# Kernel tuning notes

Measured on AMD Instinct MI355X. Metric: run time of the kernel, lower is better.

Reference implementation:

```python
import jax, jax.numpy as jnp
import numpy as np

B, N, L, D = 128, 1024, 512, 64


def setup_inputs() -> dict:
    key = jax.random.key(0)
    k1, k2 = jax.random.split(key)
    text_outputs = jax.random.normal(k1, (B, N, D), dtype=jnp.float32)
    image_outputs = jax.random.normal(k2, (B, L, D), dtype=jnp.float32)
    rng = np.random.RandomState(0)
    ntok = rng.randint(N // 4, N + 1, size=B)
    nreg = rng.randint(L // 4, L + 1, size=B)
    text_mask = (np.arange(N)[None, :] < ntok[:, None]).astype(np.float32)
    image_mask = (np.arange(L)[None, :] < nreg[:, None]).astype(np.float32)
    # impostor indices (torch code samples these with np.random inside forward;
    # here they are fixed constants for determinism), guaranteed != own index
    I_imp = rng.randint(0, B, size=B)
    S_imp = rng.randint(0, B, size=B)
    ar = np.arange(B)
    I_imp = np.where(I_imp == ar, (I_imp + 1) % B, I_imp).astype(np.int32)
    S_imp = np.where(S_imp == ar, (S_imp + 1) % B, S_imp).astype(np.int32)
    return {
        "text_outputs": text_outputs,
        "image_outputs": image_outputs,
        "text_mask": jnp.asarray(text_mask),
        "image_mask": jnp.asarray(image_mask),
        "I_imp_idx": jnp.asarray(I_imp),
        "S_imp_idx": jnp.asarray(S_imp),
    }


def _mean_max_sim(T, I, tmask, imask):
    # T: (N, D) tokens, I: (L, D) regions; masks select the ragged valid prefix.
    M = jnp.einsum('nd,ld->nl', T, I)                       # matchmap (N, L)
    neg = jnp.finfo(M.dtype).min
    mx = jnp.max(jnp.where(imask[None, :] > 0, M, neg), axis=1)  # max over regions
    return jnp.sum(mx * tmask) / jnp.sum(tmask)             # mean over valid tokens


def reference(text_outputs, image_outputs, text_mask, image_mask, I_imp_idx, S_imp_idx, margin=1.0):
    sim = jax.vmap(_mean_max_sim)
    anchor = sim(text_outputs, image_outputs, text_mask, image_mask)            # (B,)
    Simpsim = sim(text_outputs[S_imp_idx], image_outputs, text_mask[S_imp_idx], image_mask)
    Iimpsim = sim(text_outputs, image_outputs[I_imp_idx], text_mask, image_mask[I_imp_idx])
    # scalar per-sample hinge: term added only when margin+imp-anchor > 0 == relu
    per_sample = jax.nn.relu(margin + Iimpsim - anchor) + jax.nn.relu(margin + Simpsim - anchor)
    loss = jnp.sum(per_sample) / text_outputs.shape[0]
    return loss[None]  # torch returns shape (1,)
```

## Files before the change

kernel.cpp:

```cpp
#include <hip/hip_runtime.h>
#include <hip/hip_bf16.h>

#define B 128
#define N 1024
#define L 512
#define D 64
#define TT 6
#define TOKBLK 384
#define NCH 3

typedef float f32x4 __attribute__((ext_vector_type(4)));
typedef short bf16x8 __attribute__((ext_vector_type(8)));

__device__ inline bf16x8 cvt8(float4 f0, float4 f1) {
    union { __hip_bfloat162 h2[4]; bf16x8 v; } u;
    u.h2[0] = __float22bfloat162_rn(make_float2(f0.x, f0.y));
    u.h2[1] = __float22bfloat162_rn(make_float2(f0.z, f0.w));
    u.h2[2] = __float22bfloat162_rn(make_float2(f1.x, f1.y));
    u.h2[3] = __float22bfloat162_rn(make_float2(f1.z, f1.w));
    return u.v;
}

#define WS_NEED_PRE (8192 + (size_t)B * L * D * 2)

__global__ __launch_bounds__(256) void prep_kernel(
        const float* __restrict__ I, const float* __restrict__ tmask,
        const float* __restrict__ imask, unsigned short* __restrict__ Ibf,
        int* __restrict__ cnts) {
    int blk = blockIdx.x;
    int tid = threadIdx.x;
    __shared__ float red[4];
    if (blk < 1024) {
        const float* src = I + (size_t)blk * 64 * D;
        unsigned short* dst = Ibf + (size_t)blk * 4096;
#pragma unroll
        for (int j = 0; j < 2; ++j) {
            int si = tid + j * 256;
            int r = si >> 3, seg = si & 7;
            const float4* p = (const float4*)(src + (size_t)si * 8);
            bf16x8 v = cvt8(p[0], p[1]);
            int h = seg >> 2, qq = seg & 3;
            int ci = ((r >> 4) * 2 + h) * 64 + qq * 16 + (r & 15);
            *(bf16x8*)(dst + (size_t)ci * 8) = v;
        }
    } else {
        int row = blk - 1024;
        float s = 0.f;
        if (row < B) {
            const float* p = tmask + (size_t)row * N;
            for (int i = tid; i < N; i += 256) s += p[i];
        } else {
            const float* p = imask + (size_t)(row - B) * L;
            for (int i = tid; i < L; i += 256) s += p[i];
        }
        for (int off = 32; off > 0; off >>= 1) s += __shfl_down(s, off);
        if ((tid & 63) == 0) red[tid >> 6] = s;
        __syncthreads();
        if (tid == 0)
            cnts[row] = (int)(red[0] + red[1] + red[2] + red[3] + 0.5f);
    }
}

template <bool PRE>
__global__ __launch_bounds__(256, 4) void sim_kernel(
        const float* __restrict__ T, const float* __restrict__ I,
        const unsigned short* __restrict__ Ibf, const int* __restrict__ cnts,
        const int* __restrict__ Iimp, const int* __restrict__ Simp,
        float* __restrict__ partials) {
    int blk = blockIdx.x;
    int chunk = blk % NCH;
    int bs = blk / NCH;
    int b = bs & (B - 1);
    int s = bs >> 7;
    int Tb = b, Ib = b;
    if (s == 1) Tb = Simp[b];
    else if (s == 2) Ib = Iimp[b];
    int ntok = cnts[Tb];
    int nreg = cnts[B + Ib];

    int tid = threadIdx.x;
    int tok0 = chunk * TOKBLK;
    if (tok0 >= ntok) {
        if (tid == 0) partials[blk] = 0.f;
        return;
    }

    int w = tid >> 6;
    int lane = tid & 63;
    int q = lane >> 4;
    int c = lane & 15;

    __shared__ float wsum[4];

    int wt0 = tok0 + w * (TT * 16);
    bf16x8 afrag[TT][2];
#pragma unroll
    for (int tt = 0; tt < TT; ++tt) {
        int row = wt0 + tt * 16 + c;
        if (row > N - 1) row = N - 1;
        const float* trow = T + ((size_t)Tb * N + row) * D;
#pragma unroll
        for (int h = 0; h < 2; ++h) {
            const float4* p = (const float4*)(trow + h * 32 + q * 8);
            afrag[tt][h] = cvt8(p[0], p[1]);
        }
    }

    float mx[TT][4];
#pragma unroll
    for (int tt = 0; tt < TT; ++tt)
#pragma unroll
        for (int i = 0; i < 4; ++i) mx[tt][i] = -3.0e38f;

    int nrt = (nreg + 15) >> 4;
    int prem = nreg & 15;

    if (PRE) {
        const char* imgL = (const char*)(Ibf + (size_t)Ib * L * D) + (size_t)lane * 16;
        bf16x8 c0 = *(const bf16x8*)(imgL);
        bf16x8 c1 = *(const bf16x8*)(imgL + 1024);
        int r1 = (nrt > 1) ? 1 : 0;
        bf16x8 n0 = *(const bf16x8*)(imgL + (size_t)r1 * 2048);
        bf16x8 n1 = *(const bf16x8*)(imgL + (size_t)r1 * 2048 + 1024);
#pragma unroll 1
        for (int rt = 0; rt < nrt; ++rt) {
            int rp = (rt + 2 < nrt) ? rt + 2 : rt;
            const char* pp = imgL + (size_t)rp * 2048;
            bf16x8 f0 = *(const bf16x8*)(pp);
            bf16x8 f1 = *(const bf16x8*)(pp + 1024);
            bool vld = (rt + 1 < nrt) || (prem == 0) || (c < prem);
#pragma unroll
            for (int tt = 0; tt < TT; ++tt) {
                f32x4 acc = {0.f, 0.f, 0.f, 0.f};
                acc = __builtin_amdgcn_mfma_f32_16x16x32_bf16(afrag[tt][0], c0, acc, 0, 0, 0);
                acc = __builtin_amdgcn_mfma_f32_16x16x32_bf16(afrag[tt][1], c1, acc, 0, 0, 0);
                if (vld) {
#pragma unroll
                    for (int i = 0; i < 4; ++i) mx[tt][i] = fmaxf(mx[tt][i], acc[i]);
                }
            }
            c0 = n0; c1 = n1; n0 = f0; n1 = f1;
        }
    } else {
        const float* Ibase = I + (size_t)Ib * L * D;
#pragma unroll 1
        for (int rt = 0; rt < nrt; ++rt) {
            int r = rt * 16 + c;
            const float4* p0 = (const float4*)(Ibase + (size_t)r * D + q * 8);
            bf16x8 b0 = cvt8(p0[0], p0[1]);
            const float4* p1 = (const float4*)(Ibase + (size_t)r * D + 32 + q * 8);
            bf16x8 b1 = cvt8(p1[0], p1[1]);
            bool vld = (rt + 1 < nrt) || (prem == 0) || (c < prem);
#pragma unroll
            for (int tt = 0; tt < TT; ++tt) {
                f32x4 acc = {0.f, 0.f, 0.f, 0.f};
                acc = __builtin_amdgcn_mfma_f32_16x16x32_bf16(afrag[tt][0], b0, acc, 0, 0, 0);
                acc = __builtin_amdgcn_mfma_f32_16x16x32_bf16(afrag[tt][1], b1, acc, 0, 0, 0);
                if (vld) {
#pragma unroll
                    for (int i = 0; i < 4; ++i) mx[tt][i] = fmaxf(mx[tt][i], acc[i]);
                }
            }
        }
    }

#pragma unroll
    for (int m = 1; m < 16; m <<= 1) {
#pragma unroll
        for (int tt = 0; tt < TT; ++tt)
#pragma unroll
            for (int i = 0; i < 4; ++i)
                mx[tt][i] = fmaxf(mx[tt][i], __shfl_xor(mx[tt][i], m));
    }

    float bsum = 0.f;
    if (c == 0) {
#pragma unroll
        for (int tt = 0; tt < TT; ++tt)
#pragma unroll
            for (int i = 0; i < 4; ++i) {
                int row = wt0 + tt * 16 + q * 4 + i;
                if (row < ntok) bsum += mx[tt][i];
            }
    }
    for (int off = 32; off > 0; off >>= 1) bsum += __shfl_down(bsum, off);
    if (lane == 0) wsum[w] = bsum;
    __syncthreads();
    if (tid == 0)
        partials[blk] = (wsum[0] + wsum[1] + wsum[2] + wsum[3]) / (float)ntok;
}

__global__ void loss_kernel(const float* __restrict__ partials,
                            float* __restrict__ out) {
    int tid = threadIdx.x;
    __shared__ float simsL[384];
    __shared__ float w6[6];
    simsL[tid] = partials[tid * NCH] + partials[tid * NCH + 1] + partials[tid * NCH + 2];
    __syncthreads();
    float per = 0.f;
    if (tid < B) {
        float anc  = simsL[tid];
        float simp = simsL[B + tid];
        float iimp = simsL[2 * B + tid];
        per = fmaxf(1.f + iimp - anc, 0.f) + fmaxf(1.f + simp - anc, 0.f);
    }
    for (int off = 32; off > 0; off >>= 1) per += __shfl_down(per, off);
    if ((tid & 63) == 0) w6[tid >> 6] = per;
    __syncthreads();
    if (tid == 0)
        out[0] = (w6[0] + w6[1] + w6[2] + w6[3] + w6[4] + w6[5]) / (float)B;
}

extern "C" void kernel_launch(void* const* d_in, const int* in_sizes, int n_in,
                              void* d_out, int out_size, void* d_ws, size_t ws_size,
                              hipStream_t stream) {
    const float* T     = (const float*)d_in[0];
    const float* I     = (const float*)d_in[1];
    const float* tmask = (const float*)d_in[2];
    const float* imask = (const float*)d_in[3];
    const int*   Iimp  = (const int*)d_in[4];
    const int*   Simp  = (const int*)d_in[5];

    float* partials = (float*)d_ws;
    int*   cnts     = (int*)((char*)d_ws + 6144);
    unsigned short* Ibf = (unsigned short*)((char*)d_ws + 8192);

    prep_kernel<<<1024 + 2 * B, 256, 0, stream>>>(I, tmask, imask, Ibf, cnts);
    if (ws_size >= WS_NEED_PRE) {
        sim_kernel<true><<<3 * B * NCH, 256, 0, stream>>>(T, I, Ibf, cnts, Iimp, Simp, partials);
    } else {
        sim_kernel<false><<<3 * B * NCH, 256, 0, stream>>>(T, I, Ibf, cnts, Iimp, Simp, partials);
    }
    loss_kernel<<<1, 384, 0, stream>>>(partials, (float*)d_out);
}
```

Measured before the change: 128.1 us.

## Pre-convert text to bf16 fragments and split regions across waves

Result: no change. 129.5 us (+1.1%).

```diff
diff --git a/kernel.cpp b/kernel.cpp
--- a/kernel.cpp
+++ b/kernel.cpp
@@ -5,9 +5,7 @@
 #define N 1024
 #define L 512
 #define D 64
-#define TT 6
-#define TOKBLK 384
-#define NCH 3
+#define NCH 8
 
 typedef float f32x4 __attribute__((ext_vector_type(4)));
 typedef short bf16x8 __attribute__((ext_vector_type(8)));
@@ -21,18 +19,23 @@
     return u.v;
 }
 
-#define WS_NEED_PRE (8192 + (size_t)B * L * D * 2)
+#define TBF_OFF 16384
+#define IBF_OFF (16384 + 16777216)
+#define WS_NEED (IBF_OFF + (size_t)B * L * D * 2)
 
 __global__ __launch_bounds__(256) void prep_kernel(
-        const float* __restrict__ I, const float* __restrict__ tmask,
-        const float* __restrict__ imask, unsigned short* __restrict__ Ibf,
+        const float* __restrict__ T, const float* __restrict__ I,
+        const float* __restrict__ tmask, const float* __restrict__ imask,
+        unsigned short* __restrict__ Tbf, unsigned short* __restrict__ Ibf,
         int* __restrict__ cnts) {
     int blk = blockIdx.x;
     int tid = threadIdx.x;
     __shared__ float red[4];
-    if (blk < 1024) {
-        const float* src = I + (size_t)blk * 64 * D;
-        unsigned short* dst = Ibf + (size_t)blk * 4096;
+    if (blk < 3072) {
+        const float* src;
+        unsigned short* dst;
+        if (blk < 2048) { src = T + (size_t)blk * 64 * D; dst = Tbf + (size_t)blk * 4096; }
+        else { src = I + (size_t)(blk - 2048) * 64 * D; dst = Ibf + (size_t)(blk - 2048) * 4096; }
 #pragma unroll
         for (int j = 0; j < 2; ++j) {
             int si = tid + j * 256;
@@ -44,7 +47,7 @@
             *(bf16x8*)(dst + (size_t)ci * 8) = v;
         }
     } else {
-        int row = blk - 1024;
+        int row = blk - 3072;
         float s = 0.f;
         if (row < B) {
             const float* p = tmask + (size_t)row * N;
@@ -64,12 +67,13 @@
 template <bool PRE>
 __global__ __launch_bounds__(256, 4) void sim_kernel(
         const float* __restrict__ T, const float* __restrict__ I,
-        const unsigned short* __restrict__ Ibf, const int* __restrict__ cnts,
+        const unsigned short* __restrict__ Tbf, const unsigned short* __restrict__ Ibf,
+        const int* __restrict__ cnts,
         const int* __restrict__ Iimp, const int* __restrict__ Simp,
         float* __restrict__ partials) {
     int blk = blockIdx.x;
-    int chunk = blk % NCH;
-    int bs = blk / NCH;
+    int chunk = blk & (NCH - 1);
+    int bs = blk >> 3;
     int b = bs & (B - 1);
     int s = bs >> 7;
     int Tb = b, Ib = b;
@@ -79,7 +83,7 @@
     int nreg = cnts[B + Ib];
 
     int tid = threadIdx.x;
-    int tok0 = chunk * TOKBLK;
+    int tok0 = chunk * 128;
     if (tok0 >= ntok) {
         if (tid == 0) partials[blk] = 0.f;
         return;
@@ -89,105 +93,125 @@
     int lane = tid & 63;
     int q = lane >> 4;
     int c = lane & 15;
-
-    __shared__ float wsum[4];
-
-    int wt0 = tok0 + w * (TT * 16);
-    bf16x8 afrag[TT][2];
-#pragma unroll
-    for (int tt = 0; tt < TT; ++tt) {
-        int row = wt0 + tt * 16 + c;
-        if (row > N - 1) row = N - 1;
-        const float* trow = T + ((size_t)Tb * N + row) * D;
-#pragma unroll
-        for (int h = 0; h < 2; ++h) {
-            const float4* p = (const float4*)(trow + h * 32 + q * 8);
-            afrag[tt][h] = cvt8(p[0], p[1]);
-        }
-    }
-
-    float mx[TT][4];
-#pragma unroll
-    for (int tt = 0; tt < TT; ++tt)
+    int th = w >> 1;
+    int rh = w & 1;
+
+    __shared__ float ldsmx[2][2][64];
+    __shared__ float wsumS[2];
+
+    int wt0 = tok0 + th * 64;
+    bool active = wt0 < ntok;
+
+    float mx[4][4];
+#pragma unroll
+    for (int tt = 0; tt < 4; ++tt)
 #pragma unroll
         for (int i = 0; i < 4; ++i) mx[tt][i] = -3.0e38f;
 
     int nrt = (nreg + 15) >> 4;
     int prem = nreg & 15;
 
-    if (PRE) {
-        const char* imgL = (const char*)(Ibf + (size_t)Ib * L * D) + (size_t)lane * 16;
-        bf16x8 c0 = *(const bf16x8*)(imgL);
-        bf16x8 c1 = *(const bf16x8*)(imgL + 1024);
-        int r1 = (nrt > 1) ? 1 : 0;
-        bf16x8 n0 = *(const bf16x8*)(imgL + (size_t)r1 * 2048);
-        bf16x8 n1 = *(const bf16x8*)(imgL + (size_t)r1 * 2048 + 1024);
+    if (active) {
+        bf16x8 afrag[4][2];
+        if (PRE) {
+            const char* tb = (const char*)Tbf + (size_t)Tb * 131072
+                           + (size_t)(chunk * 8 + th * 4) * 2048 + (size_t)lane * 16;
+#pragma unroll
+            for (int tt = 0; tt < 4; ++tt)
+#pragma unroll
+                for (int h = 0; h < 2; ++h)
+                    afrag[tt][h] = *(const bf16x8*)(tb + tt * 2048 + h * 1024);
+        } else {
+#pragma unroll
+            for (int tt = 0; tt < 4; ++tt) {
+                const float* trow = T + ((size_t)Tb * N + wt0 + tt * 16 + c) * D;
+#pragma unroll
+                for (int h = 0; h < 2; ++h) {
+                    const float4* p = (const float4*)(trow + h * 32 + q * 8);
+                    afrag[tt][h] = cvt8(p[0], p[1]);
+                }
+            }
+        }
+
+        if (PRE) {
+            const char* imgL = (const char*)Ibf + (size_t)Ib * 65536 + (size_t)lane * 16;
+            bf16x8 c0 = {0}, c1 = {0}, n0 = {0}, n1 = {0};
+            if (rh < nrt) {
+                c0 = *(const bf16x8*)(imgL + (size_t)rh * 2048);
+                c1 = *(const bf16x8*)(imgL + (size_t)rh * 2048 + 1024);
+            }
 #pragma unroll 1
-        for (int rt = 0; rt < nrt; ++rt) {
-            int rp = (rt + 2 < nrt) ? rt + 2 : rt;
-            const char* pp = imgL + (size_t)rp * 2048;
-            bf16x8 f0 = *(const bf16x8*)(pp);
-            bf16x8 f1 = *(const bf16x8*)(pp + 1024);
-            bool vld = (rt + 1 < nrt) || (prem == 0) || (c < prem);
-#pragma unroll
-            for (int tt = 0; tt < TT; ++tt) {
-                f32x4 acc = {0.f, 0.f, 0.f, 0.f};
-                acc = __builtin_amdgcn_mfma_f32_16x16x32_bf16(afrag[tt][0], c0, acc, 0, 0, 0);
-                acc = __builtin_amdgcn_mfma_f32_16x16x32_bf16(afrag[tt][1], c1, acc, 0, 0, 0);
-                if (vld) {
-#pragma unroll
-                    for (int i = 0; i < 4; ++i) mx[tt][i] = fmaxf(mx[tt][i], acc[i]);
-                }
-            }
-            c0 = n0; c1 = n1; n0 = f0; n1 = f1;
-        }
-    } else {
-        const float* Ibase = I + (size_t)Ib * L * D;
+            for (int rt = rh; rt < nrt; rt += 2) {
+                int rn = rt + 2;
+                if (rn < nrt) {
+                    n0 = *(const bf16x8*)(imgL + (size_t)rn * 2048);
+                    n1 = *(const bf16x8*)(imgL + (size_t)rn * 2048 + 1024);
+                }
+                bool vld = (rt != nrt - 1) || (prem == 0) || (c < prem);
+#pragma unroll
+                for (int tt = 0; tt < 4; ++tt) {
+                    f32x4 acc = {0.f, 0.f, 0.f, 0.f};
+                    acc = __builtin_amdgcn_mfma_f32_16x16x32_bf16(afrag[tt][0], c0, acc, 0, 0, 0);
+                    acc = __builtin_amdgcn_mfma_f32_16x16x32_bf16(afrag[tt][1], c1, acc, 0, 0, 0);
+                    if (vld) {
+#pragma unroll
+                        for (int i = 0; i < 4; ++i) mx[tt][i] = fmaxf(mx[tt][i], acc[i]);
+                    }
+                }
+                c0 = n0; c1 = n1;
+            }
+        } else {
+            const float* Ibase = I + (size_t)Ib * L * D;
 #pragma unroll 1
-        for (int rt = 0; rt < nrt; ++rt) {
-            int r = rt * 16 + c;
-            const float4* p0 = (const float4*)(Ibase + (size_t)r * D + q * 8);
-            bf16x8 b0 = cvt8(p0[0], p0[1]);
-            const float4* p1 = (const float4*)(Ibase + (size_t)r * D + 32 + q * 8);
-            bf16x8 b1 = cvt8(p1[0], p1[1]);
-            bool vld = (rt + 1 < nrt) || (prem == 0) || (c < prem);
-#pragma unroll
-            for (int tt = 0; tt < TT; ++tt) {
-                f32x4 acc = {0.f, 0.f, 0.f, 0.f};
-                acc = __builtin_amdgcn_mfma_f32_16x16x32_bf16(afrag[tt][0], b0, acc, 0, 0, 0);
-                acc = __builtin_amdgcn_mfma_f32_16x16x32_bf16(afrag[tt][1], b1, acc, 0, 0, 0);
-                if (vld) {
-#pragma unroll
-                    for (int i = 0; i < 4; ++i) mx[tt][i] = fmaxf(mx[tt][i], acc[i]);
-                }
-            }
-        }
-    }
-
-#pragma unroll
-    for (int m = 1; m < 16; m <<= 1) {
-#pragma unroll
-        for (int tt = 0; tt < TT; ++tt)
+            for (int rt = rh; rt < nrt; rt += 2) {
+                int r = rt * 16 + c;
+                const float4* p0 = (const float4*)(Ibase + (size_t)r * D + q * 8);
+                bf16x8 b0 = cvt8(p0[0], p0[1]);
+                const float4* p1 = (const float4*)(Ibase + (size_t)r * D + 32 + q * 8);
+                bf16x8 b1 = cvt8(p1[0], p1[1]);
+                bool vld = (rt != nrt - 1) || (prem == 0) || (c < prem);
+#pragma unroll
+                for (int tt = 0; tt < 4; ++tt) {
+                    f32x4 acc = {0.f, 0.f, 0.f, 0.f};
+                    acc = __builtin_amdgcn_mfma_f32_16x16x32_bf16(afrag[tt][0], b0, acc, 0, 0, 0);
+                    acc = __builtin_amdgcn_mfma_f32_16x16x32_bf16(afrag[tt][1], b1, acc, 0, 0, 0);
+                    if (vld) {
+#pragma unroll
+                        for (int i = 0; i < 4; ++i) mx[tt][i] = fmaxf(mx[tt][i], acc[i]);
+                    }
+                }
+            }
+        }
+
+#pragma unroll
+        for (int m = 1; m < 16; m <<= 1) {
+#pragma unroll
+            for (int tt = 0; tt < 4; ++tt)
+#pragma unroll
+                for (int i = 0; i < 4; ++i)
+                    mx[tt][i] = fmaxf(mx[tt][i], __shfl_xor(mx[tt][i], m));
+        }
+    }
+
+    if (c == 0) {
+#pragma unroll
+        for (int tt = 0; tt < 4; ++tt)
 #pragma unroll
             for (int i = 0; i < 4; ++i)
-                mx[tt][i] = fmaxf(mx[tt][i], __shfl_xor(mx[tt][i], m));
-    }
-
-    float bsum = 0.f;
-    if (c == 0) {
-#pragma unroll
-        for (int tt = 0; tt < TT; ++tt)
-#pragma unroll
-            for (int i = 0; i < 4; ++i) {
-                int row = wt0 + tt * 16 + q * 4 + i;
-                if (row < ntok) bsum += mx[tt][i];
-            }
-    }
-    for (int off = 32; off > 0; off >>= 1) bsum += __shfl_down(bsum, off);
-    if (lane == 0) wsum[w] = bsum;
+                ldsmx[th][rh][tt * 16 + q * 4 + i] = mx[tt][i];
+    }
+    __syncthreads();
+
+    if (rh == 0) {
+        float v = fmaxf(ldsmx[th][0][lane], ldsmx[th][1][lane]);
+        int row = wt0 + lane;
+        float sv = (row < ntok) ? v : 0.f;
+        for (int off = 32; off > 0; off >>= 1) sv += __shfl_down(sv, off);
+        if (lane == 0) wsumS[th] = sv;
+    }
     __syncthreads();
     if (tid == 0)
-        partials[blk] = (wsum[0] + wsum[1] + wsum[2] + wsum[3]) / (float)ntok;
+        partials[blk] = (wsumS[0] + wsumS[1]) / (float)ntok;
 }
 
 __global__ void loss_kernel(const float* __restrict__ partials,
@@ -195,7 +219,11 @@
     int tid = threadIdx.x;
     __shared__ float simsL[384];
     __shared__ float w6[6];
-    simsL[tid] = partials[tid * NCH] + partials[tid * NCH + 1] + partials[tid * NCH + 2];
+    float acc = 0.f;
+    const float4* p4 = (const float4*)(partials + tid * NCH);
+    float4 v0 = p4[0], v1 = p4[1];
+    acc = (v0.x + v0.y + v0.z + v0.w) + (v1.x + v1.y + v1.z + v1.w);
+    simsL[tid] = acc;
     __syncthreads();
     float per = 0.f;
     if (tid < B) {
@@ -222,14 +250,17 @@
     const int*   Simp  = (const int*)d_in[5];
 
     float* partials = (float*)d_ws;
-    int*   cnts     = (int*)((char*)d_ws + 6144);
-    unsigned short* Ibf = (unsigned short*)((char*)d_ws + 8192);
-
-    prep_kernel<<<1024 + 2 * B, 256, 0, stream>>>(I, tmask, imask, Ibf, cnts);
-    if (ws_size >= WS_NEED_PRE) {
-        sim_kernel<true><<<3 * B * NCH, 256, 0, stream>>>(T, I, Ibf, cnts, Iimp, Simp, partials);
+    int*   cnts     = (int*)((char*)d_ws + 12288);
+    unsigned short* Tbf = (unsigned short*)((char*)d_ws + TBF_OFF);
+    unsigned short* Ibf = (unsigned short*)((char*)d_ws + IBF_OFF);
+
+    prep_kernel<<<3072 + 2 * B, 256, 0, stream>>>(T, I, tmask, imask, Tbf, Ibf, cnts);
+    if (ws_size >= WS_NEED) {
+        sim_kernel<true><<<3 * B * NCH, 256, 0, stream>>>(T, I, Tbf, Ibf, cnts,
+                                                          Iimp, Simp, partials);
     } else {
-        sim_kernel<false><<<3 * B * NCH, 256, 0, stream>>>(T, I, Ibf, cnts, Iimp, Simp, partials);
+        sim_kernel<false><<<3 * B * NCH, 256, 0, stream>>>(T, I, Tbf, Ibf, cnts,
+                                                           Iimp, Simp, partials);
     }
     loss_kernel<<<1, 384, 0, stream>>>(partials, (float*)d_out);
 }
```
